# Kernel tuning notes

Measured on AMD Instinct MI355X. Metric: run time of the kernel, lower is better.

## Reference

```python
import jax, jax.numpy as jnp
import numpy as np

THRESHOLD = 0.1      # threshold_pos; threshold_neg = -THRESHOLD (encode uses +THRESHOLD on -diff)
TIME_STEPS = 16
BETA = 4.0           # surrogate_beta for fast_sigmoid
REFRACTORY = 2       # refractory_period
EPS = 1e-8

@jax.custom_vjp
def spike_fn(v):
    # forward: hard threshold spike (0/1)
    return (v >= THRESHOLD).astype(jnp.float32)

def _spike_fwd(v):
    return spike_fn(v), v

def _spike_bwd(v, g):
    # fast-sigmoid surrogate gradient centered at threshold
    s = jax.nn.sigmoid(BETA * (v - THRESHOLD))
    return (g * BETA * s * (1.0 - s),)

spike_fn.defvjp(_spike_fwd, _spike_bwd)

def setup_inputs() -> dict:
    key = jax.random.key(0)
    cpc_features = jax.random.normal(key, (8, 4096, 128), dtype=jnp.float32)
    return {"cpc_features": cpc_features}

def reference(cpc_features):
    # cpc_features: [B, S, F] -- temporal-contrast encode each feature channel along S
    diff = jnp.diff(cpc_features, axis=1, prepend=cpc_features[:, :1, :])   # [B,S,F]
    std = jnp.std(diff, axis=1, keepdims=True)                              # [B,1,F]
    nd = diff / (std + EPS)
    pos = spike_fn(nd)      # positive-contrast spikes, [B,S,F]
    neg = spike_fn(-nd)     # negative-contrast spikes, [B,S,F]
    # refractory pattern over time steps: t%3==0 -> pos, t%3==1 -> neg, else silent
    phase = (jnp.arange(TIME_STEPS) % (REFRACTORY + 1))[None, :, None, None]  # [1,T,1,1]
    spikes = jnp.where(phase == 0, pos[:, None, :, :],
                       jnp.where(phase == 1, neg[:, None, :, :], 0.0))
    return spikes  # [B, T, S, F]
```

## Files before the change

kernel.cpp:

```cpp
#include <hip/hip_runtime.h>
#include <math.h>

typedef float f32x4 __attribute__((ext_vector_type(4)));

constexpr int kB = 8;
constexpr int kS = 4096;
constexpr int kF = 128;
constexpr int kT = 16;
constexpr int kNCHUNK = 64;
constexpr int kSCHUNK = kS / kNCHUNK;

__global__ __launch_bounds__(128) void std_partial_kernel(
    const float* __restrict__ x, double* __restrict__ psum, double* __restrict__ psq) {
    const int b = blockIdx.x / kNCHUNK;
    const int c = blockIdx.x % kNCHUNK;
    const int f = threadIdx.x;
    const long base = ((long)(b * kS + c * kSCHUNK)) * kF + f;
    float prev = (c == 0) ? x[(long)b * kS * kF + f] : x[base - kF];
    double s1 = 0.0, s2 = 0.0;
    #pragma unroll 4
    for (int j = 0; j < kSCHUNK; ++j) {
        float cur = x[base + (long)j * kF];
        float d = cur - prev;
        s1 += (double)d;
        s2 += (double)d * (double)d;
        prev = cur;
    }
    const int o = c * (kB * kF) + b * kF + f;
    psum[o] = s1;
    psq[o]  = s2;
}

__global__ __launch_bounds__(256) void std_finish_kernel(
    const double* __restrict__ psum, const double* __restrict__ psq,
    float* __restrict__ denom) {
    const int i = blockIdx.x * blockDim.x + threadIdx.x;
    if (i >= kB * kF) return;
    double s1 = 0.0, s2 = 0.0;
    #pragma unroll 8
    for (int c = 0; c < kNCHUNK; ++c) {
        s1 += psum[c * (kB * kF) + i];
        s2 += psq[c * (kB * kF) + i];
    }
    const double mean = s1 / (double)kS;
    double var = s2 / (double)kS - mean * mean;
    if (var < 0.0) var = 0.0;
    const float stdf = (float)sqrt(var);
    denom[i] = stdf + 1e-8f;
}

__global__ __launch_bounds__(128) void std_direct_kernel(
    const float* __restrict__ x, float* __restrict__ denom) {
    const int b = blockIdx.x;
    const int f = threadIdx.x;
    const long base = (long)b * kS * kF + f;
    float prev = x[base];
    double s1 = 0.0, s2 = 0.0;
    for (int s = 0; s < kS; ++s) {
        float cur = x[base + (long)s * kF];
        float d = cur - prev;
        s1 += (double)d;
        s2 += (double)d * (double)d;
        prev = cur;
    }
    const double mean = s1 / (double)kS;
    double var = s2 / (double)kS - mean * mean;
    if (var < 0.0) var = 0.0;
    denom[b * kF + f] = (float)sqrt(var) + 1e-8f;
}

__global__ __launch_bounds__(256) void spike_write_kernel(
    const float* __restrict__ x, const float* __restrict__ denom,
    float* __restrict__ out) {
    const int tid = threadIdx.x;
    const int f4 = tid & 31;
    const int sl = tid >> 5;
    const int b  = blockIdx.x >> 9;
    const int sc = blockIdx.x & 511;
    const int s  = sc * 8 + sl;

    const long inoff = ((long)(b * kS + s)) * kF + f4 * 4;
    const f32x4 cur  = *(const f32x4*)(x + inoff);
    const f32x4 prev = (s == 0) ? cur : *(const f32x4*)(x + inoff - kF);
    const f32x4 dn   = *(const f32x4*)(denom + b * kF + f4 * 4);

    f32x4 pos, neg;
    #pragma unroll
    for (int k = 0; k < 4; ++k) {
        const float d  = cur[k] - prev[k];
        const float nd = d / dn[k];
        pos[k] = (nd  >= 0.1f) ? 1.0f : 0.0f;
        neg[k] = (-nd >= 0.1f) ? 1.0f : 0.0f;
    }
    f32x4 zero;
    zero[0] = 0.0f; zero[1] = 0.0f; zero[2] = 0.0f; zero[3] = 0.0f;

    const long slice = (long)kS * kF;
    const long outbase = (((long)b * kT) * kS + s) * kF + f4 * 4;
    #pragma unroll
    for (int t = 0; t < kT; ++t) {
        const int ph = t % 3;
        const f32x4 v = (ph == 0) ? pos : ((ph == 1) ? neg : zero);
        __builtin_nontemporal_store(v, (f32x4*)(out + outbase + (long)t * slice));
    }
}

extern "C" void kernel_launch(void* const* d_in, const int* in_sizes, int n_in,
                              void* d_out, int out_size, void* d_ws, size_t ws_size,
                              hipStream_t stream) {
    const float* x = (const float*)d_in[0];
    float* out = (float*)d_out;

    float* denom = (float*)d_ws;
    double* psum = (double*)((char*)d_ws + 4096);
    double* psq  = psum + (size_t)kNCHUNK * kB * kF;
    const size_t needed = 4096 + 2ull * kNCHUNK * kB * kF * sizeof(double);

    if (ws_size >= needed) {
        std_partial_kernel<<<kB * kNCHUNK, 128, 0, stream>>>(x, psum, psq);
        std_finish_kernel<<<(kB * kF + 255) / 256, 256, 0, stream>>>(psum, psq, denom);
    } else {
        std_direct_kernel<<<kB, 128, 0, stream>>>(x, denom);
    }
    spike_write_kernel<<<kB * (kS / 8), 256, 0, stream>>>(x, denom, out);
}
```

Before: 289.8 us.

## Map one thread per output vector in linear order for spike write

Replaces the spike write kernel, which loaded each input row once and wrote 16 time-step slices, with a kernel that gives every thread one float4 output in linear memory order. The input is reloaded and recomputed for each non-silent time step, and silent steps skip the loads entirely. The aim is fully contiguous streaming stores across the grid and more parallelism. The cost is redundant input reads and divisions (about 11x) and 16x more threads.

```diff
diff --git a/kernel.cpp b/kernel.cpp
--- a/kernel.cpp
+++ b/kernel.cpp
@@ -69,40 +69,31 @@
     denom[b * kF + f] = (float)sqrt(var) + 1e-8f;
 }
 
-__global__ __launch_bounds__(256) void spike_write_kernel(
+__global__ __launch_bounds__(256) void spike_linear_kernel(
     const float* __restrict__ x, const float* __restrict__ denom,
     float* __restrict__ out) {
-    const int tid = threadIdx.x;
-    const int f4 = tid & 31;
-    const int sl = tid >> 5;
-    const int b  = blockIdx.x >> 9;
-    const int sc = blockIdx.x & 511;
-    const int s  = sc * 8 + sl;
+    const int i  = blockIdx.x * 256 + threadIdx.x;
+    const int f4 = i & 31;
+    const int s  = (i >> 5) & (kS - 1);
+    const int t  = (i >> 17) & (kT - 1);
+    const int b  = i >> 21;
+    const int ph = t % 3;
 
-    const long inoff = ((long)(b * kS + s)) * kF + f4 * 4;
-    const f32x4 cur  = *(const f32x4*)(x + inoff);
-    const f32x4 prev = (s == 0) ? cur : *(const f32x4*)(x + inoff - kF);
-    const f32x4 dn   = *(const f32x4*)(denom + b * kF + f4 * 4);
-
-    f32x4 pos, neg;
-    #pragma unroll
-    for (int k = 0; k < 4; ++k) {
-        const float d  = cur[k] - prev[k];
-        const float nd = d / dn[k];
-        pos[k] = (nd  >= 0.1f) ? 1.0f : 0.0f;
-        neg[k] = (-nd >= 0.1f) ? 1.0f : 0.0f;
+    f32x4 v;
+    v[0] = 0.0f; v[1] = 0.0f; v[2] = 0.0f; v[3] = 0.0f;
+    if (ph != 2) {
+        const long inoff = ((long)(b * kS + s)) * kF + f4 * 4;
+        const f32x4 cur  = *(const f32x4*)(x + inoff);
+        const f32x4 prev = (s == 0) ? cur : *(const f32x4*)(x + inoff - kF);
+        const f32x4 dn   = *(const f32x4*)(denom + b * kF + f4 * 4);
+        #pragma unroll
+        for (int k = 0; k < 4; ++k) {
+            const float nd = (cur[k] - prev[k]) / dn[k];
+            const float sv = (ph == 0) ? nd : -nd;
+            v[k] = (sv >= 0.1f) ? 1.0f : 0.0f;
+        }
     }
-    f32x4 zero;
-    zero[0] = 0.0f; zero[1] = 0.0f; zero[2] = 0.0f; zero[3] = 0.0f;
-
-    const long slice = (long)kS * kF;
-    const long outbase = (((long)b * kT) * kS + s) * kF + f4 * 4;
-    #pragma unroll
-    for (int t = 0; t < kT; ++t) {
-        const int ph = t % 3;
-        const f32x4 v = (ph == 0) ? pos : ((ph == 1) ? neg : zero);
-        __builtin_nontemporal_store(v, (f32x4*)(out + outbase + (long)t * slice));
-    }
+    __builtin_nontemporal_store(v, (f32x4*)(out + ((long)i << 2)));
 }
 
 extern "C" void kernel_launch(void* const* d_in, const int* in_sizes, int n_in,
@@ -122,5 +113,7 @@
     } else {
         std_direct_kernel<<<kB, 128, 0, stream>>>(x, denom);
     }
-    spike_write_kernel<<<kB * (kS / 8), 256, 0, stream>>>(x, denom, out);
+
+    const int n4 = kB * kT * kS * kF / 4;
+    spike_linear_kernel<<<n4 / 256, 256, 0, stream>>>(x, denom, out);
 }
```

New measurement: 284.5 us. About the same (-1.8%).
